# Performance work log

Hardware: AMD Instinct MI355X
Metric: run time of the kernel (lower is better)

Reference implementation:

```python
import jax, jax.numpy as jnp
import numpy as np

# --- static config (matches init_kwargs) ---
DIM = 192          # kv channels
CS = 2             # channel_scale -> q/out channels = DIM//CS
NH = 6             # num heads
WS = 4             # kv window size (q window = 2*WS)
S, H, W = 16, 32, 32          # coarse (input) resolution
SD, HD, WD = 32, 64, 64
HEAD = DIM // NH
SCALE = HEAD ** -0.5

# Relative position index: query coords are the fine-grid positions mapped to
# coarse coords via repeat_interleave(2) (as in the original coords_s/h/w),
# key coords are the coarse window positions. (Original torch code contained a
# buggy 2D->3D port of the strided key subsample; this is the consistent 3D form.)
_r = np.repeat(np.arange(WS), 2)
qc = np.stack(np.meshgrid(_r, _r, _r, indexing='ij'), -1).reshape(-1, 3)        # (512,3)
_k = np.arange(WS)
kc = np.stack(np.meshgrid(_k, _k, _k, indexing='ij'), -1).reshape(-1, 3)        # (64,3)
_rel = qc[:, None, :] - kc[None, :, :] + (WS - 1)                                # in [0, 2*WS-2]
REL_INDEX = jnp.asarray(_rel[..., 0] * (2 * WS - 1) ** 2 + _rel[..., 1] * (2 * WS - 1) + _rel[..., 2])  # (512,64)
TABLE_ROWS = (4 * WS - 1) ** 3  # as in original parameter shape


def ln(x, g, b, eps=1e-5):
    mu = jnp.mean(x, axis=-1, keepdims=True)
    var = jnp.mean(jnp.square(x - mu), axis=-1, keepdims=True)
    return (x - mu) * jax.lax.rsqrt(var + eps) * g + b


def win_part(x, ws):
    # (B,s,h,w,C) -> (B*num_windows, ws^3, C)
    B, s, h, w, C = x.shape
    x = x.reshape(B, s // ws, ws, h // ws, ws, w // ws, ws, C)
    return x.transpose(0, 1, 3, 5, 2, 4, 6, 7).reshape(-1, ws * ws * ws, C)


def win_rev(x, ws, B, s, h, w):
    # (B*num_windows, ws^3, C) -> (B,s,h,w,C)
    C = x.shape[-1]
    x = x.reshape(B, s // ws, h // ws, w // ws, ws, ws, ws, C)
    return x.transpose(0, 1, 4, 2, 5, 3, 6, 7).reshape(B, s, h, w, C)


def setup_inputs() -> dict:
    key = jax.random.key(0)
    ks = jax.random.split(key, 12)
    d = DIM
    dh = d // CS
    hid = int(dh * 4)
    f = lambda i, shape: jax.random.normal(ks[i], shape, jnp.float32) * 0.02
    return dict(
        x=jax.random.normal(ks[0], (2, S * H * W, d), jnp.float32),
        x_downsampled=jax.random.normal(ks[1], (2, SD * HD * WD, dh), jnp.float32),
        gamma1=jnp.ones((d,), jnp.float32), beta1=jnp.zeros((d,), jnp.float32),
        W_kv=f(2, (d, 2 * d)), b_kv=jnp.zeros((2 * d,), jnp.float32),
        W_q=f(3, (dh, d)), b_q=jnp.zeros((d,), jnp.float32),
        W_proj=f(4, (d, dh)), b_proj=jnp.zeros((dh,), jnp.float32),
        bias_table=f(5, (TABLE_ROWS, NH)),
        exp_gamma=jnp.ones((d,), jnp.float32), exp_beta=jnp.zeros((d,), jnp.float32),
        deconv_w=f(6, (d, dh, 2, 2, 2)), deconv_b=jnp.zeros((dh,), jnp.float32),
        gamma2=jnp.ones((dh,), jnp.float32), beta2=jnp.zeros((dh,), jnp.float32),
        W1=f(7, (dh, hid)), b1=jnp.zeros((hid,), jnp.float32),
        W2=f(8, (hid, dh)), b2=jnp.zeros((dh,), jnp.float32),
        padwh=0,
    )


def reference(x, x_downsampled, gamma1, beta1, W_kv, b_kv, W_q, b_q, W_proj, b_proj,
              bias_table, exp_gamma, exp_beta, deconv_w, deconv_b, gamma2, beta2,
              W1, b1, W2, b2, padwh):
    B = x.shape[0]
    d = DIM
    dh = d // CS
    # ---- windowed cross attention: kv from coarse x (norm1), q from fine skip ----
    kv = ln(x, gamma1, beta1).reshape(B, S, H, W, d)
    kv_w = win_part(kv, WS)                                           # (Bw, 64, d)
    q_w = win_part(x_downsampled.reshape(B, SD, HD, WD, dh), 2 * WS)  # (Bw, 512, dh)
    Bw, N, _ = kv_w.shape
    Nq = q_w.shape[1]
    kvp = kv_w @ W_kv + b_kv                                          # (Bw, N, 2d)
    k, v = jnp.split(kvp, 2, axis=-1)
    k = k.reshape(Bw, N, NH, HEAD).transpose(0, 2, 1, 3)
    v = v.reshape(Bw, N, NH, HEAD).transpose(0, 2, 1, 3)
    q = (q_w @ W_q + b_q).reshape(Bw, Nq, NH, HEAD).transpose(0, 2, 1, 3) * SCALE
    attn = jnp.einsum('bhqd,bhkd->bhqk', q, k)                        # (Bw, NH, 512, 64)
    bias = bias_table[REL_INDEX].transpose(2, 0, 1)                   # (NH, 512, 64)
    attn = jax.nn.softmax(attn + bias[None], axis=-1)
    out = jnp.einsum('bhqk,bhkd->bhqd', attn, v).transpose(0, 2, 1, 3).reshape(Bw, Nq, d)
    out = out @ W_proj + b_proj                                       # (Bw, Nq, dh)
    out = win_rev(out, 2 * WS, B, SD, HD, WD).reshape(B, SD * HD * WD, dh)
    # ---- Patch_Expanding residual: LN + ConvTranspose3d(k=2, s=2) ----
    xe = ln(x, exp_gamma, exp_beta).reshape(B, S, H, W, d)
    sc = jnp.einsum('bshwc,coijk->bsihjwko', xe, deconv_w) + deconv_b  # (B,S,2,H,2,W,2,dh)
    sc = sc.reshape(B, SD * HD * WD, dh)
    # ---- residual + MLP ----
    y = sc + out
    hdn = jax.nn.gelu(ln(y, gamma2, beta2) @ W1 + b1, approximate=False)
    return y + (hdn @ W2 + b2)
```

## Files before the change

### kernel.cpp

```cpp
#include <hip/hip_runtime.h>
#include <math.h>

#define ATT_SCALE 0.17677669529663687f

typedef __bf16 bf16x8 __attribute__((ext_vector_type(8)));
typedef __bf16 bf16x4 __attribute__((ext_vector_type(4)));
typedef float  f32x4  __attribute__((ext_vector_type(4)));

#define MFMA16(a,b,c) __builtin_amdgcn_mfma_f32_16x16x32_bf16(a,b,c,0,0,0)

#define BIAS_BYTES 786432
#define WKV_OFF 0
#define WQ_OFF  73728
#define WP_OFF  92160
#define WD_OFF  110592
#define W1_OFF  258048
#define W2_OFF  294912
#define NSWZ    331776
#define AOUT_OFF 1507328ull
#define AOUT_BYTES (262144ull * 96ull * 2ull)

static __device__ __forceinline__ float gelu_exact(float v){
    return 0.5f * v * (1.0f + erff(v * 0.70710678118654752f));
}

static __device__ __forceinline__ bf16x8 afrag(const __bf16* w, int NRT, int kt, int rt, int lane){
    return ((const bf16x8*)w)[(kt*NRT + rt)*64 + lane];
}

__global__ __launch_bounds__(256) void k_prep(const float* __restrict__ table,
    const float* __restrict__ Wkv, const float* __restrict__ Wq,
    const float* __restrict__ Wp,  const float* __restrict__ Wd,
    const float* __restrict__ W1,  const float* __restrict__ W2,
    float* __restrict__ bias, __bf16* __restrict__ wsw){
    int id = blockIdx.x * 256 + threadIdx.x;
    if (id < 196608){
        int k  = id & 63;
        int qg = (id >> 6) & 511;
        int h  = id >> 15;
        int qi = qg >> 6, qj = (qg >> 3) & 7, qk = qg & 7;
        int ki = k >> 4,  kj = (k >> 2) & 3,  kk = k & 3;
        int r0 = (qi >> 1) - ki + 3;
        int r1 = (qj >> 1) - kj + 3;
        int r2 = (qk >> 1) - kk + 3;
        bias[id] = table[((r0 * 7 + r1) * 7 + r2) * 6 + h];
        return;
    }
    id -= 196608;
    if (id >= NSWZ) return;
    if (id >= WD_OFF && id < W1_OFF){
        int lid  = id - WD_OFF;
        int j    = lid & 7, lane = (lid >> 3) & 63, tile = lid >> 9;
        int rt   = tile % 24;
        int kt2  = tile / 24;
        int ii   = kt2 / 6, kt = kt2 % 6;
        int n    = rt * 16 + (lane & 15);
        int o    = n % 96, jk = n / 96;
        int kdim = kt * 32 + (lane >> 4) * 8 + j;
        wsw[id] = (__bf16)(Wd[(kdim * 96 + o) * 8 + ii * 4 + jk]);
        return;
    }
    const float* W; int N, NRT, off; float sc = 1.f;
    if      (id < WQ_OFF){ W = Wkv; N = 384; NRT = 24; off = WKV_OFF; }
    else if (id < WP_OFF){ W = Wq;  N = 192; NRT = 12; off = WQ_OFF; sc = ATT_SCALE; }
    else if (id < WD_OFF){ W = Wp;  N = 96;  NRT = 6;  off = WP_OFF; }
    else if (id < W2_OFF){ W = W1;  N = 384; NRT = 24; off = W1_OFF; }
    else                 { W = W2;  N = 96;  NRT = 6;  off = W2_OFF; }
    int lid  = id - off;
    int j    = lid & 7, lane = (lid >> 3) & 63, tile = lid >> 9;
    int rt   = tile % NRT, kt = tile / NRT;
    int n    = rt * 16 + (lane & 15);
    int k    = kt * 32 + (lane >> 4) * 8 + j;
    wsw[id + 0] = (__bf16)(W[k * N + n] * sc);
}

__global__ __launch_bounds__(512) void k_attn(const float* __restrict__ x,
    const float* __restrict__ xd, const float* __restrict__ g1, const float* __restrict__ b1v,
    const float* __restrict__ bkv, const float* __restrict__ bq, const float* __restrict__ bpj,
    const __bf16* __restrict__ wsw, const float* __restrict__ bias, float* __restrict__ yout,
    __bf16* __restrict__ aout){
    __shared__ __bf16 Qs[64][196];
    __shared__ __bf16 Ks[64][196];
    __shared__ __bf16 Vt[192][68];
    __shared__ __bf16 Wqp_s[36864];
    const int tid = threadIdx.x, lane = tid & 63, w = tid >> 6;
    const int win = blockIdx.x, b = win >> 8, wrem = win & 255;
    const int sw_ = wrem >> 6, hw_ = (wrem >> 3) & 7, ww_ = wrem & 7;

    #pragma unroll
    for (int i = 0; i < 9; i++)
        ((uint4*)Wqp_s)[tid + 512*i] = ((const uint4*)(wsw + WQ_OFF))[tid + 512*i];

    {
        int row = tid >> 3, sub = tid & 7;
        int si = row >> 4, hi = (row >> 2) & 3, wi = row & 3;
        int ci = ((b * 16 + 4 * sw_ + si) * 32 + 4 * hw_ + hi) * 32 + 4 * ww_ + wi;
        const float* xp = x + ci * 192 + sub * 24;
        float v[24]; float s = 0.f, ss = 0.f;
        #pragma unroll
        for (int i = 0; i < 6; i++){
            float4 t = ((const float4*)xp)[i];
            v[4*i] = t.x; v[4*i+1] = t.y; v[4*i+2] = t.z; v[4*i+3] = t.w;
            s += t.x + t.y + t.z + t.w;
            ss += t.x*t.x + t.y*t.y + t.z*t.z + t.w*t.w;
        }
        #pragma unroll
        for (int m = 1; m < 8; m <<= 1){ s += __shfl_xor(s, m); ss += __shfl_xor(ss, m); }
        float mu = s * (1.f/192.f), var = ss * (1.f/192.f) - mu*mu, rs = rsqrtf(var + 1e-5f);
        #pragma unroll
        for (int i = 0; i < 3; i++){
            bf16x8 t;
            #pragma unroll
            for (int jj = 0; jj < 8; jj++){
                int c = sub*24 + 8*i + jj;
                t[jj] = (__bf16)((v[8*i+jj] - mu) * rs * g1[c] + b1v[c]);
            }
            *(bf16x8*)&Qs[row][sub*24 + 8*i] = t;
        }
    }
    __syncthreads();
    {
        const int ct = w & 3, rh = w >> 2;
        const int tok = ct * 16 + (lane & 15);
        bf16x8 bfr[6];
        #pragma unroll
        for (int kt = 0; kt < 6; kt++) bfr[kt] = *(const bf16x8*)&Qs[tok][kt*32 + (lane>>4)*8];
        #pragma unroll
        for (int i = 0; i < 12; i++){
            int rt = rh * 12 + i;
            f32x4 acc = {0.f,0.f,0.f,0.f};
            #pragma unroll
            for (int kt = 0; kt < 6; kt++) acc = MFMA16(afrag(wsw + WKV_OFF, 24, kt, rt, lane), bfr[kt], acc);
            int cb = rt * 16 + ((lane >> 4) << 2);
            float4 b4 = *(const float4*)&bkv[cb];
            acc[0] += b4.x; acc[1] += b4.y; acc[2] += b4.z; acc[3] += b4.w;
            if (cb < 192){
                bf16x4 t;
                #pragma unroll
                for (int r = 0; r < 4; r++) t[r] = (__bf16)acc[r];
                *(bf16x4*)&Ks[tok][cb] = t;
            } else {
                #pragma unroll
                for (int r = 0; r < 4; r++) Vt[cb - 192 + r][tok] = (__bf16)acc[r];
            }
        }
    }
    __syncthreads();

    const int li_ = lane & 15, gt_ = lane >> 4, rsel = lane >> 5;

    for (int qt = 0; qt < 8; qt++){
        {
            const int ct = w & 3, rh = w >> 2;
            const int ql = ct * 16 + (lane & 15);
            const int ft = ((b * 32 + 8 * sw_ + qt) * 64 + 8 * hw_ + (ql >> 3)) * 64 + 8 * ww_ + (ql & 7);
            bf16x8 bfr[3];
            #pragma unroll
            for (int kt = 0; kt < 3; kt++){
                const float* xp = xd + ft * 96 + kt * 32 + (lane >> 4) * 8;
                float4 t0 = *(const float4*)xp;
                float4 t1 = *(const float4*)(xp + 4);
                bf16x8 t;
                t[0]=(__bf16)t0.x; t[1]=(__bf16)t0.y; t[2]=(__bf16)t0.z; t[3]=(__bf16)t0.w;
                t[4]=(__bf16)t1.x; t[5]=(__bf16)t1.y; t[6]=(__bf16)t1.z; t[7]=(__bf16)t1.w;
                bfr[kt] = t;
            }
            #pragma unroll
            for (int i = 0; i < 6; i++){
                int rt = rh * 6 + i;
                f32x4 acc = {0.f,0.f,0.f,0.f};
                #pragma unroll
                for (int kt = 0; kt < 3; kt++) acc = MFMA16(afrag(Wqp_s, 12, kt, rt, lane), bfr[kt], acc);
                int cb = rt * 16 + ((lane >> 4) << 2);
                float4 b4 = *(const float4*)&bq[cb];
                bf16x4 t;
                t[0] = (__bf16)(acc[0] + b4.x * ATT_SCALE);
                t[1] = (__bf16)(acc[1] + b4.y * ATT_SCALE);
                t[2] = (__bf16)(acc[2] + b4.z * ATT_SCALE);
                t[3] = (__bf16)(acc[3] + b4.w * ATT_SCALE);
                *(bf16x4*)&Qs[ql][cb] = t;
            }
        }
        __syncthreads();
        f32x4 ov[3][2];
        #pragma unroll
        for (int ui = 0; ui < 3; ui++){
            const int u = w * 3 + ui;
            const int h = u >> 2, qct = u & 3;
            f32x4 sc[4];
            __builtin_amdgcn_s_setprio(1);
            #pragma unroll
            for (int rt = 0; rt < 4; rt++){
                bf16x8 a  = *(const bf16x8*)&Ks[rt*16 + li_][h*32 + gt_*8];
                bf16x8 bq8 = *(const bf16x8*)&Qs[qct*16 + li_][h*32 + gt_*8];
                f32x4 z = {0.f,0.f,0.f,0.f};
                sc[rt] = MFMA16(a, bq8, z);
            }
            __builtin_amdgcn_s_setprio(0);
            const int qg = qt * 64 + qct * 16 + li_;
            const float* bp = bias + (h * 512 + qg) * 64 + (gt_ << 2);
            #pragma unroll
            for (int rt = 0; rt < 4; rt++){
                float4 b4 = *(const float4*)(bp + rt * 16);
                sc[rt][0] += b4.x; sc[rt][1] += b4.y; sc[rt][2] += b4.z; sc[rt][3] += b4.w;
            }
            float m = sc[0][0];
            #pragma unroll
            for (int rt = 0; rt < 4; rt++)
                #pragma unroll
                for (int r = 0; r < 4; r++) m = fmaxf(m, sc[rt][r]);
            m = fmaxf(m, __shfl_xor(m, 16));
            m = fmaxf(m, __shfl_xor(m, 32));
            float sum = 0.f;
            #pragma unroll
            for (int rt = 0; rt < 4; rt++)
                #pragma unroll
                for (int r = 0; r < 4; r++){ float e = __expf(sc[rt][r] - m); sc[rt][r] = e; sum += e; }
            sum += __shfl_xor(sum, 16);
            sum += __shfl_xor(sum, 32);
            float inv = 1.f / sum;
            unsigned pwv[4][2];
            #pragma unroll
            for (int rt = 0; rt < 4; rt++){
                union { __bf16 hh[2]; unsigned u; } c0, c1;
                c0.hh[0] = (__bf16)(sc[rt][0] * inv); c0.hh[1] = (__bf16)(sc[rt][1] * inv);
                c1.hh[0] = (__bf16)(sc[rt][2] * inv); c1.hh[1] = (__bf16)(sc[rt][3] * inv);
                pwv[rt][0] = c0.u; pwv[rt][1] = c1.u;
            }
            unsigned bfw[2][4];
            #pragma unroll
            for (int kt = 0; kt < 2; kt++){
                #pragma unroll
                for (int t = 0; t < 4; t++){
                    int gs   = ((gt_ & 1) << 1) + (t >> 1);
                    int addr = (((gs << 4) + li_) << 2);
                    int w0 = __builtin_amdgcn_ds_bpermute(addr, (int)pwv[2*kt + 0][t & 1]);
                    int w1 = __builtin_amdgcn_ds_bpermute(addr, (int)pwv[2*kt + 1][t & 1]);
                    bfw[kt][t] = rsel ? (unsigned)w1 : (unsigned)w0;
                }
            }
            union { unsigned u[4]; bf16x8 v; } pb0, pb1;
            #pragma unroll
            for (int t = 0; t < 4; t++){ pb0.u[t] = bfw[0][t]; pb1.u[t] = bfw[1][t]; }
            __builtin_amdgcn_s_setprio(1);
            #pragma unroll
            for (int dt = 0; dt < 2; dt++){
                f32x4 o = {0.f,0.f,0.f,0.f};
                bf16x8 a0 = *(const bf16x8*)&Vt[h*32 + dt*16 + li_][gt_*8];
                bf16x8 a1 = *(const bf16x8*)&Vt[h*32 + dt*16 + li_][32 + gt_*8];
                o = MFMA16(a0, pb0.v, o);
                o = MFMA16(a1, pb1.v, o);
                ov[ui][dt] = o;
            }
            __builtin_amdgcn_s_setprio(0);
        }
        __syncthreads();
        #pragma unroll
        for (int ui = 0; ui < 3; ui++){
            const int u = w * 3 + ui;
            const int h = u >> 2, qct = u & 3;
            const int tok = qct * 16 + li_;
            #pragma unroll
            for (int dt = 0; dt < 2; dt++){
                int cb = h * 32 + dt * 16 + (gt_ << 2);
                bf16x4 t;
                #pragma unroll
                for (int r = 0; r < 4; r++) t[r] = (__bf16)ov[ui][dt][r];
                *(bf16x4*)&Qs[tok][cb] = t;
            }
        }
        __syncthreads();
        {
            const int ct = w & 3, rh = w >> 2;
            const int ql = ct * 16 + (lane & 15);
            const int ft = ((b * 32 + 8 * sw_ + qt) * 64 + 8 * hw_ + (ql >> 3)) * 64 + 8 * ww_ + (ql & 7);
            bf16x8 bfr[6];
            #pragma unroll
            for (int kt = 0; kt < 6; kt++) bfr[kt] = *(const bf16x8*)&Qs[ql][kt*32 + (lane>>4)*8];
            #pragma unroll
            for (int i = 0; i < 3; i++){
                int rt = rh * 3 + i;
                f32x4 acc = {0.f,0.f,0.f,0.f};
                #pragma unroll
                for (int kt = 0; kt < 6; kt++) acc = MFMA16(afrag(Wqp_s + 18432, 6, kt, rt, lane), bfr[kt], acc);
                int cb = rt * 16 + ((lane >> 4) << 2);
                float4 b4 = *(const float4*)&bpj[cb];
                float4 res;
                res.x = acc[0] + b4.x;
                res.y = acc[1] + b4.y;
                res.z = acc[2] + b4.z;
                res.w = acc[3] + b4.w;
                if (aout){
                    bf16x4 tb;
                    tb[0] = (__bf16)res.x; tb[1] = (__bf16)res.y;
                    tb[2] = (__bf16)res.z; tb[3] = (__bf16)res.w;
                    *(bf16x4*)&aout[ft * 96 + cb] = tb;
                } else {
                    *(float4*)&yout[ft * 96 + cb] = res;
                }
            }
        }
        __syncthreads();
    }
}

__global__ __launch_bounds__(512) void k_mlp(const float* __restrict__ x,
    const float* __restrict__ eg, const float* __restrict__ eb,
    const float* __restrict__ g2, const float* __restrict__ b2v,
    const __bf16* __restrict__ wsw, const float* __restrict__ db,
    const float* __restrict__ b1m, const float* __restrict__ b2m,
    float* __restrict__ outp, const __bf16* __restrict__ ain){
    __shared__ __bf16 xe[32][200];
    __shared__ __bf16 ybf[64][100];
    __shared__ __bf16 yln[64][104];
    __shared__ __bf16 hsm[64][104];
    const int tid = threadIdx.x, lane = tid & 63, w = tid >> 6;
    const int t0 = blockIdx.x * 64;
    const int bb   = t0 >> 17;
    const int sbar = (t0 >> 12) & 31;
    const int hbar = (t0 >> 6) & 63;
    const int iD = sbar & 1, jD = hbar & 1;
    const int sc_ = sbar >> 1, hc_ = hbar >> 1;

    float4 apf[3];
    {
        int rowP = tid >> 3, subP = tid & 7;
        if (ain){
            const __bf16* ap = ain + (t0 + rowP) * 96 + subP * 12;
            #pragma unroll
            for (int i2 = 0; i2 < 3; i2++){
                bf16x4 a4 = ((const bf16x4*)ap)[i2];
                apf[i2].x = (float)a4[0]; apf[i2].y = (float)a4[1];
                apf[i2].z = (float)a4[2]; apf[i2].w = (float)a4[3];
            }
        } else {
            const float* ap = outp + (t0 + rowP) * 96 + subP * 12;
            apf[0] = ((const float4*)ap)[0];
            apf[1] = ((const float4*)ap)[1];
            apf[2] = ((const float4*)ap)[2];
        }
    }

    {
        int row = tid >> 4, sub = tid & 15;
        int ci = ((bb * 16 + sc_) * 32 + hc_) * 32 + row;
        const float* xp = x + ci * 192 + sub * 12;
        float v[12]; float s = 0.f, ss = 0.f;
        #pragma unroll
        for (int i2 = 0; i2 < 3; i2++){
            float4 t = ((const float4*)xp)[i2];
            v[4*i2] = t.x; v[4*i2+1] = t.y; v[4*i2+2] = t.z; v[4*i2+3] = t.w;
            s += t.x + t.y + t.z + t.w;
            ss += t.x*t.x + t.y*t.y + t.z*t.z + t.w*t.w;
        }
        #pragma unroll
        for (int m = 1; m < 16; m <<= 1){ s += __shfl_xor(s, m); ss += __shfl_xor(ss, m); }
        float mu = s * (1.f/192.f), var = ss * (1.f/192.f) - mu*mu, rs = rsqrtf(var + 1e-5f);
        #pragma unroll
        for (int i2 = 0; i2 < 3; i2++){
            bf16x4 t;
            #pragma unroll
            for (int jj = 0; jj < 4; jj++){
                int c = sub*12 + 4*i2 + jj;
                t[jj] = (__bf16)((v[4*i2+jj] - mu) * rs * eg[c] + eb[c]);
            }
            *(bf16x4*)&xe[row][sub*12 + 4*i2] = t;
        }
    }
    __syncthreads();
    {
        const int li = lane & 15, gt = lane >> 4;
        const int ctD = w & 1, rhD = w >> 1;
        const int wcol = ctD * 16 + li;
        bf16x8 bfrD[6];
        #pragma unroll
        for (int kt = 0; kt < 6; kt++) bfrD[kt] = *(const bf16x8*)&xe[wcol][kt*32 + gt*8];
        const __bf16* wd = wsw + WD_OFF + iD * 73728;
        #pragma unroll
        for (int i2 = 0; i2 < 3; i2++){
            int rtl = rhD * 3 + i2;
            int rt  = 12 * jD + rtl;
            f32x4 acc = {0.f,0.f,0.f,0.f};
            #pragma unroll
            for (int kt = 0; kt < 6; kt++) acc = MFMA16(afrag(wd, 24, kt, rt, lane), bfrD[kt], acc);
            int mp   = rtl * 16 + (gt << 2);
            int kpar = (mp >= 96) ? 1 : 0;
            int o    = mp - 96 * kpar;
            int tok  = 2 * wcol + kpar;
            float4 d4 = *(const float4*)&db[o];
            bf16x4 t;
            t[0] = (__bf16)(acc[0] + d4.x); t[1] = (__bf16)(acc[1] + d4.y);
            t[2] = (__bf16)(acc[2] + d4.z); t[3] = (__bf16)(acc[3] + d4.w);
            *(bf16x4*)&ybf[tok][o] = t;
        }
    }
    __syncthreads();
    {
        int row = tid >> 3, sub = tid & 7;
        float v[12]; float s = 0.f, ss = 0.f;
        #pragma unroll
        for (int i2 = 0; i2 < 3; i2++){
            float4 t = apf[i2];
            bf16x4 s4 = *(const bf16x4*)&ybf[row][sub*12 + 4*i2];
            t.x += (float)s4[0]; t.y += (float)s4[1];
            t.z += (float)s4[2]; t.w += (float)s4[3];
            v[4*i2] = t.x; v[4*i2+1] = t.y; v[4*i2+2] = t.z; v[4*i2+3] = t.w;
            s += t.x + t.y + t.z + t.w;
            ss += t.x*t.x + t.y*t.y + t.z*t.z + t.w*t.w;
            bf16x4 yb;
            yb[0] = (__bf16)t.x; yb[1] = (__bf16)t.y;
            yb[2] = (__bf16)t.z; yb[3] = (__bf16)t.w;
            *(bf16x4*)&ybf[row][sub*12 + 4*i2] = yb;
        }
        #pragma unroll
        for (int m = 1; m < 8; m <<= 1){ s += __shfl_xor(s, m); ss += __shfl_xor(ss, m); }
        float mu = s * (1.f/96.f), var = ss * (1.f/96.f) - mu*mu, rs = rsqrtf(var + 1e-5f);
        #pragma unroll
        for (int i2 = 0; i2 < 3; i2++){
            bf16x4 t;
            #pragma unroll
            for (int jj = 0; jj < 4; jj++){
                int c = sub*12 + 4*i2 + jj;
                t[jj] = (__bf16)((v[4*i2+jj] - mu) * rs * g2[c] + b2v[c]);
            }
            *(bf16x4*)&yln[row][sub*12 + 4*i2] = t;
        }
    }
    __syncthreads();
    const int ct = w & 3, rh = w >> 2;
    const int tok = ct * 16 + (lane & 15);
    bf16x8 bfrY[3];
    #pragma unroll
    for (int kt = 0; kt < 3; kt++) bfrY[kt] = *(const bf16x8*)&yln[tok][kt*32 + (lane>>4)*8];
    f32x4 oacc[3];
    #pragma unroll
    for (int i = 0; i < 3; i++){ f32x4 z = {0.f,0.f,0.f,0.f}; oacc[i] = z; }

    #pragma unroll
    for (int ch = 0; ch < 4; ch++){
        #pragma unroll
        for (int i = 0; i < 3; i++){
            int rtl = rh * 3 + i;
            int rtg = ch * 6 + rtl;
            f32x4 acc = {0.f,0.f,0.f,0.f};
            #pragma unroll
            for (int kt = 0; kt < 3; kt++) acc = MFMA16(afrag(wsw + W1_OFF, 24, kt, rtg, lane), bfrY[kt], acc);
            int cb = rtl * 16 + ((lane >> 4) << 2);
            float4 b4 = *(const float4*)&b1m[ch * 96 + cb];
            bf16x4 t;
            t[0] = (__bf16)gelu_exact(acc[0] + b4.x);
            t[1] = (__bf16)gelu_exact(acc[1] + b4.y);
            t[2] = (__bf16)gelu_exact(acc[2] + b4.z);
            t[3] = (__bf16)gelu_exact(acc[3] + b4.w);
            *(bf16x4*)&hsm[tok][cb] = t;
        }
        __syncthreads();
        bf16x8 bfrH[3];
        #pragma unroll
        for (int kt = 0; kt < 3; kt++) bfrH[kt] = *(const bf16x8*)&hsm[tok][kt*32 + (lane>>4)*8];
        #pragma unroll
        for (int i = 0; i < 3; i++){
            int rt = rh * 3 + i;
            #pragma unroll
            for (int kt = 0; kt < 3; kt++)
                oacc[i] = MFMA16(afrag(wsw + W2_OFF, 6, ch * 3 + kt, rt, lane), bfrH[kt], oacc[i]);
        }
        __syncthreads();
    }
    #pragma unroll
    for (int i = 0; i < 3; i++){
        int rt = rh * 3 + i;
        int cb = rt * 16 + ((lane >> 4) << 2);
        float4 b4 = *(const float4*)&b2m[cb];
        bf16x4 yv = *(const bf16x4*)&ybf[tok][cb];
        float4 res;
        res.x = (float)yv[0] + oacc[i][0] + b4.x;
        res.y = (float)yv[1] + oacc[i][1] + b4.y;
        res.z = (float)yv[2] + oacc[i][2] + b4.z;
        res.w = (float)yv[3] + oacc[i][3] + b4.w;
        *(float4*)&outp[(t0 + tok) * 96 + cb] = res;
    }
}

extern "C" void kernel_launch(void* const* d_in, const int* in_sizes, int n_in,
                              void* d_out, int out_size, void* d_ws, size_t ws_size,
                              hipStream_t stream){
    const float* x    = (const float*)d_in[0];
    const float* xd   = (const float*)d_in[1];
    const float* g1   = (const float*)d_in[2];
    const float* b1v  = (const float*)d_in[3];
    const float* Wkv  = (const float*)d_in[4];
    const float* bkv  = (const float*)d_in[5];
    const float* Wq   = (const float*)d_in[6];
    const float* bq   = (const float*)d_in[7];
    const float* Wp   = (const float*)d_in[8];
    const float* bpj  = (const float*)d_in[9];
    const float* btab = (const float*)d_in[10];
    const float* eg   = (const float*)d_in[11];
    const float* eb   = (const float*)d_in[12];
    const float* dw   = (const float*)d_in[13];
    const float* db   = (const float*)d_in[14];
    const float* g2   = (const float*)d_in[15];
    const float* b2v  = (const float*)d_in[16];
    const float* W1   = (const float*)d_in[17];
    const float* b1m  = (const float*)d_in[18];
    const float* W2   = (const float*)d_in[19];
    const float* b2m  = (const float*)d_in[20];
    (void)in_sizes; (void)n_in; (void)out_size;

    float*   out  = (float*)d_out;
    float*   bias = (float*)d_ws;
    __bf16*  wsw  = (__bf16*)((char*)d_ws + BIAS_BYTES);
    __bf16*  aout = (ws_size >= AOUT_OFF + AOUT_BYTES)
                    ? (__bf16*)((char*)d_ws + AOUT_OFF) : (__bf16*)nullptr;

    k_prep<<<2064, 256, 0, stream>>>(btab, Wkv, Wq, Wp, dw, W1, W2, bias, wsw);
    k_attn<<<512, 512, 0, stream>>>(x, xd, g1, b1v, bkv, bq, bpj, wsw, bias, out, aout);
    k_mlp <<<4096, 512, 0, stream>>>(x, eg, eb, g2, b2v, wsw, db, b1m, b2m, out, aout);
}
```

Measured before the change: 294.3 us.

## Add separate output buffer, fuse next-tile Q projection with out-projection, drop barriers

Adds a dedicated shared Os buffer so attention outputs are written directly from registers instead of staged after a barrier into Qs. Out-projection for tile qt and Q projection for tile qt+1 now share one phase, cutting per-iteration barriers from four to two. Only the Q weights are kept in LDS; the projection weights are read from global memory. This frees the LDS taken by the second weight half but adds global or L2 reads of Wp every tile.

```diff
diff --git a/kernel.cpp b/kernel.cpp
--- a/kernel.cpp
+++ b/kernel.cpp
@@ -80,16 +80,17 @@
     const __bf16* __restrict__ wsw, const float* __restrict__ bias, float* __restrict__ yout,
     __bf16* __restrict__ aout){
     __shared__ __bf16 Qs[64][196];
+    __shared__ __bf16 Os[64][196];
     __shared__ __bf16 Ks[64][196];
     __shared__ __bf16 Vt[192][68];
-    __shared__ __bf16 Wqp_s[36864];
+    __shared__ __bf16 Wq_s[18432];
     const int tid = threadIdx.x, lane = tid & 63, w = tid >> 6;
     const int win = blockIdx.x, b = win >> 8, wrem = win & 255;
     const int sw_ = wrem >> 6, hw_ = (wrem >> 3) & 7, ww_ = wrem & 7;
 
     #pragma unroll
     for (int i = 0; i < 9; i++)
-        ((uint4*)Wqp_s)[tid + 512*i] = ((const uint4*)(wsw + WQ_OFF))[tid + 512*i];
+        ((uint2*)Wq_s)[tid + 512*i] = ((const uint2*)(wsw + WQ_OFF))[tid + 512*i];
 
     {
         int row = tid >> 3, sub = tid & 7;
@@ -148,41 +149,72 @@
     __syncthreads();
 
     const int li_ = lane & 15, gt_ = lane >> 4, rsel = lane >> 5;
+    const int ctQ = w & 3, rhQ = w >> 2;
+    const int qlQ = ctQ * 16 + li_;
+
+    auto qproj = [&](int qt){
+        const int ft = ((b * 32 + 8 * sw_ + qt) * 64 + 8 * hw_ + (qlQ >> 3)) * 64 + 8 * ww_ + (qlQ & 7);
+        bf16x8 bfr[3];
+        #pragma unroll
+        for (int kt = 0; kt < 3; kt++){
+            const float* xp = xd + ft * 96 + kt * 32 + gt_ * 8;
+            float4 t0 = *(const float4*)xp;
+            float4 t1 = *(const float4*)(xp + 4);
+            bf16x8 t;
+            t[0]=(__bf16)t0.x; t[1]=(__bf16)t0.y; t[2]=(__bf16)t0.z; t[3]=(__bf16)t0.w;
+            t[4]=(__bf16)t1.x; t[5]=(__bf16)t1.y; t[6]=(__bf16)t1.z; t[7]=(__bf16)t1.w;
+            bfr[kt] = t;
+        }
+        #pragma unroll
+        for (int i = 0; i < 6; i++){
+            int rt = rhQ * 6 + i;
+            f32x4 acc = {0.f,0.f,0.f,0.f};
+            #pragma unroll
+            for (int kt = 0; kt < 3; kt++) acc = MFMA16(afrag(Wq_s, 12, kt, rt, lane), bfr[kt], acc);
+            int cb = rt * 16 + (gt_ << 2);
+            float4 b4 = *(const float4*)&bq[cb];
+            bf16x4 t;
+            t[0] = (__bf16)(acc[0] + b4.x * ATT_SCALE);
+            t[1] = (__bf16)(acc[1] + b4.y * ATT_SCALE);
+            t[2] = (__bf16)(acc[2] + b4.z * ATT_SCALE);
+            t[3] = (__bf16)(acc[3] + b4.w * ATT_SCALE);
+            *(bf16x4*)&Qs[qlQ][cb] = t;
+        }
+    };
+
+    auto outproj = [&](int qt){
+        const int ft = ((b * 32 + 8 * sw_ + qt) * 64 + 8 * hw_ + (qlQ >> 3)) * 64 + 8 * ww_ + (qlQ & 7);
+        bf16x8 bfr[6];
+        #pragma unroll
+        for (int kt = 0; kt < 6; kt++) bfr[kt] = *(const bf16x8*)&Os[qlQ][kt*32 + gt_*8];
+        #pragma unroll
+        for (int i = 0; i < 3; i++){
+            int rt = rhQ * 3 + i;
+            f32x4 acc = {0.f,0.f,0.f,0.f};
+            #pragma unroll
+            for (int kt = 0; kt < 6; kt++) acc = MFMA16(afrag(wsw + WP_OFF, 6, kt, rt, lane), bfr[kt], acc);
+            int cb = rt * 16 + (gt_ << 2);
+            float4 b4 = *(const float4*)&bpj[cb];
+            float4 res;
+            res.x = acc[0] + b4.x;
+            res.y = acc[1] + b4.y;
+            res.z = acc[2] + b4.z;
+            res.w = acc[3] + b4.w;
+            if (aout){
+                bf16x4 tb;
+                tb[0] = (__bf16)res.x; tb[1] = (__bf16)res.y;
+                tb[2] = (__bf16)res.z; tb[3] = (__bf16)res.w;
+                *(bf16x4*)&aout[ft * 96 + cb] = tb;
+            } else {
+                *(float4*)&yout[ft * 96 + cb] = res;
+            }
+        }
+    };
+
+    qproj(0);
+    __syncthreads();
 
     for (int qt = 0; qt < 8; qt++){
-        {
-            const int ct = w & 3, rh = w >> 2;
-            const int ql = ct * 16 + (lane & 15);
-            const int ft = ((b * 32 + 8 * sw_ + qt) * 64 + 8 * hw_ + (ql >> 3)) * 64 + 8 * ww_ + (ql & 7);
-            bf16x8 bfr[3];
-            #pragma unroll
-            for (int kt = 0; kt < 3; kt++){
-                const float* xp = xd + ft * 96 + kt * 32 + (lane >> 4) * 8;
-                float4 t0 = *(const float4*)xp;
-                float4 t1 = *(const float4*)(xp + 4);
-                bf16x8 t;
-                t[0]=(__bf16)t0.x; t[1]=(__bf16)t0.y; t[2]=(__bf16)t0.z; t[3]=(__bf16)t0.w;
-                t[4]=(__bf16)t1.x; t[5]=(__bf16)t1.y; t[6]=(__bf16)t1.z; t[7]=(__bf16)t1.w;
-                bfr[kt] = t;
-            }
-            #pragma unroll
-            for (int i = 0; i < 6; i++){
-                int rt = rh * 6 + i;
-                f32x4 acc = {0.f,0.f,0.f,0.f};
-                #pragma unroll
-                for (int kt = 0; kt < 3; kt++) acc = MFMA16(afrag(Wqp_s, 12, kt, rt, lane), bfr[kt], acc);
-                int cb = rt * 16 + ((lane >> 4) << 2);
-                float4 b4 = *(const float4*)&bq[cb];
-                bf16x4 t;
-                t[0] = (__bf16)(acc[0] + b4.x * ATT_SCALE);
-                t[1] = (__bf16)(acc[1] + b4.y * ATT_SCALE);
-                t[2] = (__bf16)(acc[2] + b4.z * ATT_SCALE);
-                t[3] = (__bf16)(acc[3] + b4.w * ATT_SCALE);
-                *(bf16x4*)&Qs[ql][cb] = t;
-            }
-        }
-        __syncthreads();
-        f32x4 ov[3][2];
         #pragma unroll
         for (int ui = 0; ui < 3; ui++){
             const int u = w * 3 + ui;
@@ -250,56 +282,18 @@
                 bf16x8 a1 = *(const bf16x8*)&Vt[h*32 + dt*16 + li_][32 + gt_*8];
                 o = MFMA16(a0, pb0.v, o);
                 o = MFMA16(a1, pb1.v, o);
-                ov[ui][dt] = o;
-            }
-            __builtin_amdgcn_s_setprio(0);
-        }
-        __syncthreads();
-        #pragma unroll
-        for (int ui = 0; ui < 3; ui++){
-            const int u = w * 3 + ui;
-            const int h = u >> 2, qct = u & 3;
-            const int tok = qct * 16 + li_;
-            #pragma unroll
-            for (int dt = 0; dt < 2; dt++){
+                const int tok = qct * 16 + li_;
                 int cb = h * 32 + dt * 16 + (gt_ << 2);
                 bf16x4 t;
                 #pragma unroll
-                for (int r = 0; r < 4; r++) t[r] = (__bf16)ov[ui][dt][r];
-                *(bf16x4*)&Qs[tok][cb] = t;
-            }
+                for (int r = 0; r < 4; r++) t[r] = (__bf16)o[r];
+                *(bf16x4*)&Os[tok][cb] = t;
+            }
+            __builtin_amdgcn_s_setprio(0);
         }
         __syncthreads();
-        {
-            const int ct = w & 3, rh = w >> 2;
-            const int ql = ct * 16 + (lane & 15);
-            const int ft = ((b * 32 + 8 * sw_ + qt) * 64 + 8 * hw_ + (ql >> 3)) * 64 + 8 * ww_ + (ql & 7);
-            bf16x8 bfr[6];
-            #pragma unroll
-            for (int kt = 0; kt < 6; kt++) bfr[kt] = *(const bf16x8*)&Qs[ql][kt*32 + (lane>>4)*8];
-            #pragma unroll
-            for (int i = 0; i < 3; i++){
-                int rt = rh * 3 + i;
-                f32x4 acc = {0.f,0.f,0.f,0.f};
-                #pragma unroll
-                for (int kt = 0; kt < 6; kt++) acc = MFMA16(afrag(Wqp_s + 18432, 6, kt, rt, lane), bfr[kt], acc);
-                int cb = rt * 16 + ((lane >> 4) << 2);
-                float4 b4 = *(const float4*)&bpj[cb];
-                float4 res;
-                res.x = acc[0] + b4.x;
-                res.y = acc[1] + b4.y;
-                res.z = acc[2] + b4.z;
-                res.w = acc[3] + b4.w;
-                if (aout){
-                    bf16x4 tb;
-                    tb[0] = (__bf16)res.x; tb[1] = (__bf16)res.y;
-                    tb[2] = (__bf16)res.z; tb[3] = (__bf16)res.w;
-                    *(bf16x4*)&aout[ft * 96 + cb] = tb;
-                } else {
-                    *(float4*)&yout[ft * 96 + cb] = res;
-                }
-            }
-        }
+        outproj(qt);
+        if (qt < 7) qproj(qt + 1);
         __syncthreads();
     }
 }
```

Result: no change. 293.6 us (-0.3%).
